# Optimization experiments

Hardware: AMD Instinct MI355X
Metric: run time of the kernel (lower is better)

The kernel has to match this reference:

```python
import jax, jax.numpy as jnp
import numpy as np

SPEC_WINDOW = 32
SPEC_HOP = 8
PELT_PENALTY = 3.0
PATCH_MIN = 8
PATCH_MAX = 64
PATCH_GRID = 2
ANCHOR_LEN = 16
ALPHA = 1.0
BETA = 1.0


def _spectral_batch_np(segs):
    # segs: [N, L] -> (feat [N,3], dom_period [N], bandwidth [N])
    segs = np.asarray(segs, dtype=np.float64)
    n, L = segs.shape
    if L < 2:
        return (np.zeros((n, 3), np.float32), np.ones(n, np.float32), np.zeros(n, np.float32))
    power = np.abs(np.fft.rfft(segs, axis=-1)) ** 2
    p = power[:, 1:]  # drop DC
    if p.shape[1] < 1:
        return (np.zeros((n, 3), np.float32), np.ones(n, np.float32), np.zeros(n, np.float32))
    total = p.sum(-1)
    probs = p / (total[:, None] + 1e-12)
    K = p.shape[1]
    freqs = np.arange(1, K + 1, dtype=np.float64) / L
    centroid = (probs * freqs).sum(-1)
    spread = np.sqrt(np.maximum((probs * (freqs - centroid[:, None]) ** 2).sum(-1), 0.0))
    dom_idx = p.argmax(-1)
    dom_period = L / (dom_idx + 1.0)
    bandwidth = 2.0 * spread  # normalized spectral spread
    feat = np.stack([centroid, bandwidth, np.log1p(total / L)], -1)
    return feat.astype(np.float32), dom_period.astype(np.float32), bandwidth.astype(np.float32)


def _dp_changepoints(feat, penalty):
    # penalized least-squares segmentation over window features
    feat = np.asarray(feat, np.float64)
    n, d = feat.shape
    cs = np.vstack([np.zeros((1, d)), np.cumsum(feat, 0)])
    cs2 = np.vstack([np.zeros((1, d)), np.cumsum(feat * feat, 0)])
    Fv = np.full(n + 1, np.inf)
    Fv[0] = 0.0
    parent = np.zeros(n + 1, np.int64)
    for t in range(1, n + 1):
        seglen = np.arange(t, 0, -1, dtype=np.float64)
        ds = cs[t] - cs[:t]
        ds2 = cs2[t] - cs2[:t]
        cost = ds2.sum(-1) - (ds * ds).sum(-1) / seglen
        vals = Fv[:t] + cost + penalty
        j = int(np.argmin(vals))
        Fv[t] = vals[j]
        parent[t] = j
    b = [n]
    t = n
    while t > 0:
        t = int(parent[t])
        b.append(t)
    return b[::-1]


def _detect_boundaries(agg):
    L = agg.shape[0]
    if L <= max(2, PATCH_MIN):
        return [0, L]
    window = min(SPEC_WINDOW, L)
    if L <= window:
        starts = [0]
        wins = agg[None, :]
    else:
        wins = np.lib.stride_tricks.sliding_window_view(agg, window)[::SPEC_HOP]
        starts = list(range(0, L - window + 1, SPEC_HOP))
        if starts[-1] != L - window:
            starts.append(L - window)
            wins = np.concatenate([wins, agg[None, -window:]], 0)
    feat, _, _ = _spectral_batch_np(wins)
    if feat.shape[0] <= 1:
        return [0, L]
    wb = _dp_changepoints(feat, PELT_PENALTY)
    bounds = [0]
    for w in wb[1:-1]:
        if w < 0 or w >= len(starts):
            continue
        t_idx = int(starts[w])
        if t_idx <= bounds[-1]:
            continue
        if t_idx - bounds[-1] < PATCH_MIN:
            continue
        if L - t_idx < PATCH_MIN:
            continue
        bounds.append(t_idx)
    bounds.append(L)
    return bounds


def _segment_stats(seg):
    if seg.shape[0] < 2:
        return 1.0, 0.0
    _, dp, bw = _spectral_batch_np(seg[None, :])
    return float(dp[0]), float(bw[0])


def _gen_patch_len(dom_period, bandwidth, seg_len):
    raw = ALPHA * dom_period / (1.0 + BETA * bandwidth)
    p = int(round(raw / PATCH_GRID)) * PATCH_GRID
    return max(1, max(PATCH_MIN, min(PATCH_MAX, p)))


def _plan_sample(series):
    # series: np [C, L]; returns (ops, starts, ends, regimes)
    C, L = series.shape
    agg = series.mean(0)
    bounds = _detect_boundaries(agg)
    ops = []
    starts = []
    ends = []
    regimes = []
    for s, e in zip(bounds[:-1], bounds[1:]):
        if e <= s:
            continue
        dp, bw = _segment_stats(agg[s:e])
        pl = _gen_patch_len(dp, bw, e - s)
        regime = (dp / max(L, 1), bw, (e - s) / max(L, 1))
        n_full = (e - s) // pl
        full_len = n_full * pl
        if n_full > 0:
            ops.append(("full", s, n_full, pl))
            starts += [s + i * pl for i in range(n_full)]
            ends += [s + (i + 1) * pl for i in range(n_full)]
            regimes += [regime] * n_full
        if full_len < e - s:
            ops.append(("tail", s + full_len, e))
            starts.append(s + full_len)
            ends.append(e)
            regimes.append(regime)
    if not ops:
        dp, bw = _segment_stats(agg)
        ops.append(("tail", 0, L))
        starts = [0]
        ends = [L]
        regimes = [(dp / max(L, 1), bw, 1.0)]
    return ops, np.asarray(starts, np.int64), np.asarray(ends, np.int64), np.asarray(regimes, np.float32)


def _lin_resize(arr, out_len):
    # matches F.interpolate(mode='linear', align_corners=False) on last dim
    P = arr.shape[-1]
    if P == out_len:
        return arr
    pos = (jnp.arange(out_len, dtype=jnp.float32) + 0.5) * (P / out_len) - 0.5
    pos = jnp.clip(pos, 0.0, P - 1)
    i0 = jnp.floor(pos).astype(jnp.int32)
    i1 = jnp.minimum(i0 + 1, P - 1)
    w = (pos - i0.astype(jnp.float32)).astype(arr.dtype)
    return arr[..., i0] * (1 - w) + arr[..., i1] * w


def _extract(xb, ops):
    # xb: jnp [C, L] -> [n_tokens, C, ANCHOR_LEN]
    C = xb.shape[0]
    chunks = []
    for op in ops:
        if op[0] == "full":
            _, s, n_full, pl = op
            full = xb[:, s:s + n_full * pl].reshape(C, n_full, pl).transpose(1, 0, 2)
            chunks.append(_lin_resize(full, ANCHOR_LEN))
        else:
            _, s, e = op
            chunks.append(_lin_resize(xb[:, s:e], ANCHOR_LEN)[None])
    return jnp.concatenate(chunks, 0)


def setup_inputs() -> dict:
    key = jax.random.key(0)
    x = jax.random.normal(key, (32, 64, 8192), dtype=jnp.float32)
    return {"x": x}


def reference(x):
    B, C, L = x.shape
    x_np = np.asarray(x)
    plans = [_plan_sample(x_np[b]) for b in range(B)]
    n_tok = [p[1].shape[0] for p in plans]
    N = max(n_tok)
    dc = float(max(L - 1, 1))
    ds = float(max(L, 1))
    patches = jnp.zeros((B, N, C, ANCHOR_LEN), jnp.float32)
    mask = np.zeros((B, N), bool)
    so = np.zeros((B, N), np.int64)
    eo = np.zeros((B, N), np.int64)
    co = np.zeros((B, N, 1), np.float32)
    sp = np.zeros((B, N, 1), np.float32)
    rg = np.zeros((B, N, 3), np.float32)
    for b, (ops, st, en, regime) in enumerate(plans):
        pb = _extract(x[b], ops)
        n = st.shape[0]
        patches = patches.at[b, :n].set(pb)
        mask[b, :n] = True
        so[b, :n] = st
        eo[b, :n] = en
        co[b, :n, 0] = ((st + en - 1.0) * 0.5 / dc).astype(np.float32)
        sp[b, :n, 0] = ((en - st) / ds).astype(np.float32)
        rg[b, :n] = regime
    return (patches, jnp.asarray(mask), jnp.asarray(so), jnp.asarray(eo), jnp.asarray(co), jnp.asarray(sp), jnp.asarray(rg), jnp.asarray(np.asarray(n_tok, np.int64)))
```

## Files before the change

kernel.cpp:

```cpp
#include <hip/hip_runtime.h>
#include <math.h>

#define BB 32
#define CC 64
#define LL 8192
#define WIN 32
#define HOP 8
#define NW 1021
#define NT 1022
#define NBINS 4096
#define SEGSTRIDE 1024
#define OFFSTRIDE 1025
#define MAXTOK 2048
#define ANCH 16
#define TWO_PI 6.283185307179586476925286766559
#define DP_TILE 64
#define DP_WAVES 8

__global__ void k_agg(const float* __restrict__ x, float* __restrict__ agg) {
  int idx = blockIdx.x * blockDim.x + threadIdx.x;
  if (idx >= BB * LL) return;
  int b = idx / LL, l = idx - b * LL;
  const float* xp = x + (size_t)b * CC * LL + l;
  float acc = 0.0f;
  for (int c = 0; c < CC; ++c) acc += xp[(size_t)c * LL];
  agg[idx] = acc / 64.0f;
}

__global__ void k_winfeat(const float* __restrict__ agg, float* __restrict__ feat) {
  __shared__ double ct[32], st[32];
  int b = blockIdx.x;
  int w = blockIdx.y * blockDim.x + threadIdx.x;
  if (threadIdx.x < 32) {
    double ang = -TWO_PI * (double)threadIdx.x / 32.0;
    sincos(ang, &st[threadIdx.x], &ct[threadIdx.x]);
  }
  __syncthreads();
  if (w >= NW) return;
  const float* a = agg + b * LL + w * HOP;
  double p[17];
  for (int k = 1; k <= 16; ++k) {
    double re = 0.0, im = 0.0;
    int m = 0;
    for (int n = 0; n < 32; ++n) {
      double av = (double)a[n];
      re += av * ct[m];
      im += av * st[m];
      m = (m + k) & 31;
    }
    p[k] = re * re + im * im;
  }
  double r[8];
  for (int j = 0; j < 8; ++j) r[j] = p[1 + j] + p[9 + j];
  double total = ((r[0] + r[1]) + (r[2] + r[3])) + ((r[4] + r[5]) + (r[6] + r[7]));
  double denom = total + 1e-12;
  double probs[17];
  for (int k = 1; k <= 16; ++k) probs[k] = p[k] / denom;
  for (int j = 0; j < 8; ++j)
    r[j] = probs[1 + j] * ((double)(1 + j) / 32.0) + probs[9 + j] * ((double)(9 + j) / 32.0);
  double centroid = ((r[0] + r[1]) + (r[2] + r[3])) + ((r[4] + r[5]) + (r[6] + r[7]));
  for (int j = 0; j < 8; ++j) {
    double f0 = (double)(1 + j) / 32.0 - centroid;
    double f1 = (double)(9 + j) / 32.0 - centroid;
    r[j] = probs[1 + j] * (f0 * f0) + probs[9 + j] * (f1 * f1);
  }
  double var = ((r[0] + r[1]) + (r[2] + r[3])) + ((r[4] + r[5]) + (r[6] + r[7]));
  double spread = sqrt(fmax(var, 0.0));
  size_t fo = ((size_t)b * 1024 + w) * 3;
  feat[fo + 0] = (float)centroid;
  feat[fo + 1] = (float)(2.0 * spread);
  feat[fo + 2] = (float)log1p(total / 32.0);
}

__global__ void __launch_bounds__(512)
k_dp(const float* __restrict__ feat,
     int* __restrict__ seg_s, int* __restrict__ seg_e,
     int* __restrict__ nsegp, int* __restrict__ segoff, int* __restrict__ binseg) {
  int b = blockIdx.x, tid = threadIdx.x;
  int wv = tid >> 6, lane = tid & 63;
  __shared__ double cs[NT][3];
  __shared__ double q[NT];
  __shared__ double G[NT];
  __shared__ short parent[NT];
  __shared__ int soff[OFFSTRIDE];
  __shared__ double redv[DP_WAVES][DP_TILE];
  __shared__ int redi[DP_WAVES][DP_TILE];
  __shared__ int ns_sh;

  if (tid == 0) {
    cs[0][0] = 0.0; cs[0][1] = 0.0; cs[0][2] = 0.0;
    q[0] = 0.0; G[0] = 0.0;
  }
  if (tid < 6) {
    int d = tid % 3; bool sq = tid >= 3;
    double acc = 0.0;
    for (int i = 0; i < NW; ++i) {
      double v = (double)feat[((size_t)b * 1024 + i) * 3 + d];
      acc += sq ? v * v : v;
      if (!sq) cs[i + 1][d] = acc;
      double a4 = __shfl(acc, 4);
      double a5 = __shfl(acc, 5);
      if (tid == 3) q[i + 1] = (acc + a4) + a5;
    }
  }
  __syncthreads();

  const int ntiles = (NW + DP_TILE - 1) / DP_TILE;
  for (int g = 0; g < ntiles; ++g) {
    int T0 = g * DP_TILE;
    int tcount = NW - T0; if (tcount > DP_TILE) tcount = DP_TILE;
    int t = T0 + 1 + lane;
    bool tvalid = lane < tcount;
    double ct0 = 0.0, ct1 = 0.0, ct2 = 0.0, Qt3 = 0.0;
    if (tvalid) { ct0 = cs[t][0]; ct1 = cs[t][1]; ct2 = cs[t][2]; Qt3 = q[t] + 3.0; }

    int njp = T0 + 1;
    int chunk = (njp + DP_WAVES - 1) / DP_WAVES;
    int j0 = wv * chunk;
    int j1 = j0 + chunk; if (j1 > njp) j1 = njp;
    double bv = INFINITY; int bj = 0x7fffffff;
    for (int j = j0; j < j1; ++j) {
      double c0 = cs[j][0], c1 = cs[j][1], c2 = cs[j][2], Gj = G[j];
      double d0 = ct0 - c0, d1 = ct1 - c1, d2 = ct2 - c2;
      double dd = (d0 * d0 + d1 * d1) + d2 * d2;
      double val = (Gj + Qt3) - dd / (double)(t - j);
      if (val < bv) { bv = val; bj = j; }
    }
    redv[wv][lane] = bv; redi[wv][lane] = bj;
    __syncthreads();

    if (wv == 0) {
      bv = redv[0][lane]; bj = redi[0][lane];
      for (int w = 1; w < DP_WAVES; ++w) {
        double ov = redv[w][lane]; int oj = redi[w][lane];
        if (ov < bv || (ov == bv && oj < bj)) { bv = ov; bj = oj; }
      }
      for (int l2 = 0; l2 < tcount - 1; ++l2) {
        double Gj_self = bv - (Qt3 - 3.0);
        double Gj  = __shfl(Gj_self, l2);
        double cj0 = __shfl(ct0, l2);
        double cj1 = __shfl(ct1, l2);
        double cj2 = __shfl(ct2, l2);
        if (tvalid && lane > l2) {
          double d0 = ct0 - cj0, d1 = ct1 - cj1, d2 = ct2 - cj2;
          double dd = (d0 * d0 + d1 * d1) + d2 * d2;
          double val = (Gj + Qt3) - dd / (double)(lane - l2);
          if (val < bv) { bv = val; bj = T0 + 1 + l2; }
        }
      }
      if (tvalid) { parent[t] = (short)bj; G[t] = bv - (Qt3 - 3.0); }
    }
    __syncthreads();
  }

  if (tid == 0) {
    short* path = (short*)&q[0];
    int* sb = (int*)&G[0];
    int cnt = 0, t = NW;
    while (t > 0) { t = parent[t]; path[cnt++] = (short)t; }
    int nb = 0, prev = 0;
    sb[nb++] = 0;
    for (int i = cnt - 2; i >= 0; --i) {
      int w = path[i];
      int ti = w * HOP;
      if (ti <= prev) continue;
      if (ti - prev < 8) continue;
      if (LL - ti < 8) continue;
      sb[nb++] = ti; prev = ti;
    }
    sb[nb++] = LL;
    int ns = nb - 1;
    ns_sh = ns;
    nsegp[b] = ns;
    int off = 0;
    for (int i = 0; i < ns; ++i) { soff[i] = off; off += (sb[i + 1] - sb[i]) >> 1; }
    soff[ns] = off;
  }
  __syncthreads();
  int ns = ns_sh;
  const int* sb = (const int*)&G[0];
  for (int i = tid; i < ns; i += 512) {
    seg_s[b * SEGSTRIDE + i] = sb[i];
    seg_e[b * SEGSTRIDE + i] = sb[i + 1];
    segoff[b * OFFSTRIDE + i] = soff[i];
    int o0 = soff[i], o1 = soff[i + 1];
    for (int qq = o0; qq < o1; ++qq) binseg[b * NBINS + qq] = i;
  }
  if (tid == 0) segoff[b * OFFSTRIDE + ns] = soff[ns];
}

__global__ void __launch_bounds__(256)
k_power(const float* __restrict__ agg,
        const int* __restrict__ seg_s, const int* __restrict__ seg_e,
        const int* __restrict__ segoff, const int* __restrict__ binseg,
        double* __restrict__ powb) {
  int gid = blockIdx.x * 256 + threadIdx.x;
  int lane8 = gid & 7;
  int bino = gid >> 3;
  int b = bino >> 12;
  int bin = bino & (NBINS - 1);
  int seg = binseg[b * NBINS + bin];
  int s = seg_s[b * SEGSTRIDE + seg];
  int e = seg_e[b * SEGSTRIDE + seg];
  int Ls = e - s;
  int k = bin - segoff[b * OFFSTRIDE + seg] + 1;
  const float* a = agg + b * LL + s;
  double wr, wi;
  sincos(-TWO_PI * (double)(8 * k) / (double)Ls, &wi, &wr);
  double cr, ci;
  sincos(-TWO_PI * (double)(k * lane8) / (double)Ls, &ci, &cr);
  double re = 0.0, im = 0.0;
  int j = 0;
  for (int n = lane8; n < Ls; n += 8, ++j) {
    if ((j & 63) == 0 && j) {
      int m = (int)(((long long)k * n) % Ls);
      sincos(-TWO_PI * (double)m / (double)Ls, &ci, &cr);
    }
    double av = (double)a[n];
    re = fma(av, cr, re);
    im = fma(av, ci, im);
    double nr = cr * wr - ci * wi;
    ci = fma(cr, wi, ci * wr);
    cr = nr;
  }
  for (int off = 4; off; off >>= 1) {
    re += __shfl_down(re, off, 8);
    im += __shfl_down(im, off, 8);
  }
  if (lane8 == 0) powb[(size_t)b * NBINS + bin] = re * re + im * im;
}

__global__ void k_segstat(const double* __restrict__ powb,
                          const int* __restrict__ seg_s, const int* __restrict__ seg_e,
                          const int* __restrict__ segoff, const int* __restrict__ nsegp,
                          float* __restrict__ dpv, float* __restrict__ bwv,
                          int* __restrict__ plv, int* __restrict__ ntokv) {
  int b = blockIdx.x, sidx = blockIdx.y;
  if (sidx >= nsegp[b]) return;
  int lane = threadIdx.x;
  int s = seg_s[b * SEGSTRIDE + sidx], e = seg_e[b * SEGSTRIDE + sidx];
  int Ls = e - s;
  int K = Ls >> 1;
  const double* p = powb + (size_t)b * NBINS + segoff[b * OFFSTRIDE + sidx];
  double T = 0.0, mx = -1.0; int mi = 0x7fffffff;
  for (int j = lane; j < K; j += 64) {
    double pv = p[j];
    T += pv;
    if (pv > mx) { mx = pv; mi = j; }
  }
  for (int off = 32; off > 0; off >>= 1) {
    T += __shfl_down(T, off);
    double omx = __shfl_down(mx, off);
    int omi = __shfl_down(mi, off);
    if (omx > mx || (omx == mx && omi < mi)) { mx = omx; mi = omi; }
  }
  T = __shfl(T, 0); mi = __shfl(mi, 0);
  double denom = T + 1e-12;
  double cp = 0.0;
  for (int j = lane; j < K; j += 64) cp += p[j] * ((double)(j + 1) / (double)Ls);
  for (int off = 32; off > 0; off >>= 1) cp += __shfl_down(cp, off);
  double c = __shfl(cp, 0) / denom;
  double sp2 = 0.0;
  for (int j = lane; j < K; j += 64) {
    double d = (double)(j + 1) / (double)Ls - c;
    sp2 += p[j] * (d * d);
  }
  for (int off = 32; off > 0; off >>= 1) sp2 += __shfl_down(sp2, off);
  if (lane == 0) {
    double spread = sqrt(fmax(sp2 / denom, 0.0));
    float dp32 = (float)((double)Ls / ((double)mi + 1.0));
    float bw32 = (float)(2.0 * spread);
    double raw = (double)dp32 / (1.0 + (double)bw32);
    int pl = (int)rint(raw * 0.5) * 2;
    pl = pl < 8 ? 8 : (pl > 64 ? 64 : pl);
    int nf = Ls / pl;
    dpv[b * SEGSTRIDE + sidx] = dp32;
    bwv[b * SEGSTRIDE + sidx] = bw32;
    plv[b * SEGSTRIDE + sidx] = pl;
    ntokv[b * SEGSTRIDE + sidx] = nf + ((nf * pl < Ls) ? 1 : 0);
  }
}

__global__ void k_plan(const int* __restrict__ nsegp, const int* __restrict__ ntokv,
                       const int* __restrict__ plv,
                       const int* __restrict__ seg_s, const int* __restrict__ seg_e,
                       int* __restrict__ tok_st, int* __restrict__ tok_en,
                       int* __restrict__ tok_sg, int* __restrict__ ntok,
                       float* __restrict__ out_ntok) {
  int b = blockIdx.x, tid = threadIdx.x;
  __shared__ int toff[SEGSTRIDE];
  int ns = nsegp[b];
  if (tid == 0) {
    int acc = 0;
    for (int i = 0; i < ns; ++i) { toff[i] = acc; acc += ntokv[b * SEGSTRIDE + i]; }
    if (acc > MAXTOK) acc = MAXTOK;
    ntok[b] = acc;
    out_ntok[b] = (float)acc;
  }
  __syncthreads();
  for (int i = tid; i < ns; i += blockDim.x) {
    int base = toff[i];
    int s = seg_s[b * SEGSTRIDE + i], e = seg_e[b * SEGSTRIDE + i];
    int pl = plv[b * SEGSTRIDE + i];
    int Ls = e - s;
    int nf = Ls / pl;
    for (int t = 0; t < nf; ++t) {
      int g = base + t;
      if (g >= MAXTOK) break;
      tok_st[b * MAXTOK + g] = s + t * pl;
      tok_en[b * MAXTOK + g] = s + (t + 1) * pl;
      tok_sg[b * MAXTOK + g] = i;
    }
    if (nf * pl < Ls) {
      int g = base + nf;
      if (g < MAXTOK) {
        tok_st[b * MAXTOK + g] = s + nf * pl;
        tok_en[b * MAXTOK + g] = e;
        tok_sg[b * MAXTOK + g] = i;
      }
    }
  }
}

__global__ void k_meta(const int* __restrict__ ntok,
                       const int* __restrict__ tok_st, const int* __restrict__ tok_en,
                       const int* __restrict__ tok_sg,
                       const float* __restrict__ dpv, const float* __restrict__ bwv,
                       const int* __restrict__ seg_s, const int* __restrict__ seg_e,
                       float* __restrict__ out, int N) {
  int idx = blockIdx.x * blockDim.x + threadIdx.x;
  if (idx >= BB * N) return;
  int b = idx / N, n = idx - b * N;
  float mask = 0, so = 0, eo = 0, co = 0, sp = 0, r0 = 0, r1 = 0, r2 = 0;
  if (n < ntok[b]) {
    int st = tok_st[b * MAXTOK + n], en = tok_en[b * MAXTOK + n], sg = tok_sg[b * MAXTOK + n];
    mask = 1.0f;
    so = (float)st; eo = (float)en;
    co = (float)(((double)st + (double)en - 1.0) * 0.5 / 8191.0);
    sp = (float)((double)(en - st) / 8192.0);
    r0 = (float)((double)dpv[b * SEGSTRIDE + sg] / 8192.0);
    r1 = bwv[b * SEGSTRIDE + sg];
    r2 = (float)((double)(seg_e[b * SEGSTRIDE + sg] - seg_s[b * SEGSTRIDE + sg]) / 8192.0);
  }
  size_t Nz = (size_t)N;
  size_t o1 = (size_t)32768 * Nz;
  out[o1 + idx] = mask;
  out[o1 + 32 * Nz + idx] = so;
  out[o1 + 64 * Nz + idx] = eo;
  out[o1 + 96 * Nz + idx] = co;
  out[o1 + 128 * Nz + idx] = sp;
  size_t o6 = o1 + 160 * Nz;
  out[o6 + (size_t)idx * 3 + 0] = r0;
  out[o6 + (size_t)idx * 3 + 1] = r1;
  out[o6 + (size_t)idx * 3 + 2] = r2;
}

__global__ void k_patches(const float* __restrict__ x,
                          const int* __restrict__ ntok,
                          const int* __restrict__ tok_st, const int* __restrict__ tok_en,
                          float* __restrict__ out, int N) {
  int blk = blockIdx.x;
  int b = blk / N, n = blk - b * N;
  size_t obase = (size_t)blk * (CC * ANCH);
  if (n >= ntok[b]) {
    for (int i = threadIdx.x; i < CC * ANCH; i += blockDim.x) out[obase + i] = 0.0f;
    return;
  }
  int st = tok_st[b * MAXTOK + n], en = tok_en[b * MAXTOK + n];
  int P = en - st;
  float scale = (float)((double)P / 16.0);
  float hi = (float)(P - 1);
  const float* xb = x + (size_t)b * CC * LL + st;
  for (int i = threadIdx.x; i < CC * ANCH; i += blockDim.x) {
    int c = i >> 4, k = i & 15;
    float pos = ((float)k + 0.5f) * scale - 0.5f;
    pos = fminf(fmaxf(pos, 0.0f), hi);
    int i0 = (int)floorf(pos);
    int i1 = min(i0 + 1, P - 1);
    float wgt = pos - (float)i0;
    const float* row = xb + (size_t)c * LL;
    out[obase + i] = row[i0] * (1.0f - wgt) + row[i1] * wgt;
  }
}

extern "C" void kernel_launch(void* const* d_in, const int* in_sizes, int n_in,
                              void* d_out, int out_size, void* d_ws, size_t ws_size,
                              hipStream_t stream) {
  const float* x = (const float*)d_in[0];
  float* out = (float*)d_out;
  int N = (out_size - BB) / 33024;
  if (N <= 0) return;

  char* ws = (char*)d_ws;
  size_t o = 0;
  auto A = [&](size_t bytes) { size_t r = o; o += (bytes + 255) & ~(size_t)255; return r; };
  float*  agg    = (float*) (ws + A((size_t)BB * LL * 4));
  float*  feat   = (float*) (ws + A((size_t)BB * 1024 * 3 * 4));
  int*    seg_s  = (int*)   (ws + A((size_t)BB * SEGSTRIDE * 4));
  int*    seg_e  = (int*)   (ws + A((size_t)BB * SEGSTRIDE * 4));
  int*    segoff = (int*)   (ws + A((size_t)BB * OFFSTRIDE * 4));
  int*    binseg = (int*)   (ws + A((size_t)BB * NBINS * 4));
  int*    nsegp  = (int*)   (ws + A((size_t)BB * 4));
  double* powb   = (double*)(ws + A((size_t)BB * NBINS * 8));
  float*  dpv    = (float*) (ws + A((size_t)BB * SEGSTRIDE * 4));
  float*  bwv    = (float*) (ws + A((size_t)BB * SEGSTRIDE * 4));
  int*    plv    = (int*)   (ws + A((size_t)BB * SEGSTRIDE * 4));
  int*    ntokv  = (int*)   (ws + A((size_t)BB * SEGSTRIDE * 4));
  int*    tok_st = (int*)   (ws + A((size_t)BB * MAXTOK * 4));
  int*    tok_en = (int*)   (ws + A((size_t)BB * MAXTOK * 4));
  int*    tok_sg = (int*)   (ws + A((size_t)BB * MAXTOK * 4));
  int*    ntok   = (int*)   (ws + A((size_t)BB * 4));
  (void)ws_size; (void)in_sizes; (void)n_in;

  k_agg<<<dim3((BB * LL + 255) / 256), dim3(256), 0, stream>>>(x, agg);
  k_winfeat<<<dim3(BB, (NW + 255) / 256), dim3(256), 0, stream>>>(agg, feat);
  k_dp<<<dim3(BB), dim3(512), 0, stream>>>(feat, seg_s, seg_e, nsegp, segoff, binseg);
  k_power<<<dim3(BB * NBINS * 8 / 256), dim3(256), 0, stream>>>(agg, seg_s, seg_e, segoff, binseg, powb);
  k_segstat<<<dim3(BB, SEGSTRIDE), dim3(64), 0, stream>>>(powb, seg_s, seg_e, segoff, nsegp,
                                                          dpv, bwv, plv, ntokv);
  k_plan<<<dim3(BB), dim3(256), 0, stream>>>(nsegp, ntokv, plv, seg_s, seg_e,
                                             tok_st, tok_en, tok_sg, ntok,
                                             out + (size_t)33024 * N);
  k_meta<<<dim3((BB * N + 255) / 256), dim3(256), 0, stream>>>(ntok, tok_st, tok_en, tok_sg,
                                                               dpv, bwv, seg_s, seg_e, out, N);
  k_patches<<<dim3(BB * N), dim3(256), 0, stream>>>(x, ntok, tok_st, tok_en, out, N);
}
```

Before: 1.408 ms.

## Split segment DFT into radix-8 sub-DFTs plus twiddle combine pass

Replaces the direct per-bin DFT over each segment with a two-stage radix-8 decimation-in-time scheme. The first kernel computes length-Ls/8 DFTs of each residue class, and the second combines the eight sub-results with twiddles per bin. This cuts the trig-recurrence arithmetic per bin by roughly the radix factor. In exchange it adds a per-sample segment map, an extra workspace buffer and launch, and relies on segment lengths being multiples of eight. It falls back to the old kernel when the workspace is too small.

```diff
diff --git a/kernel.cpp b/kernel.cpp
--- a/kernel.cpp
+++ b/kernel.cpp
@@ -75,7 +75,8 @@
 __global__ void __launch_bounds__(512)
 k_dp(const float* __restrict__ feat,
      int* __restrict__ seg_s, int* __restrict__ seg_e,
-     int* __restrict__ nsegp, int* __restrict__ segoff, int* __restrict__ binseg) {
+     int* __restrict__ nsegp, int* __restrict__ segoff, int* __restrict__ binseg,
+     int* __restrict__ smap) {
   int b = blockIdx.x, tid = threadIdx.x;
   int wv = tid >> 6, lane = tid & 63;
   __shared__ double cs[NT][3];
@@ -185,15 +186,18 @@
     segoff[b * OFFSTRIDE + i] = soff[i];
     int o0 = soff[i], o1 = soff[i + 1];
     for (int qq = o0; qq < o1; ++qq) binseg[b * NBINS + qq] = i;
+    if (smap) {
+      for (int p = sb[i]; p < sb[i + 1]; ++p) smap[b * LL + p] = i;
+    }
   }
   if (tid == 0) segoff[b * OFFSTRIDE + ns] = soff[ns];
 }
 
 __global__ void __launch_bounds__(256)
-k_power(const float* __restrict__ agg,
-        const int* __restrict__ seg_s, const int* __restrict__ seg_e,
-        const int* __restrict__ segoff, const int* __restrict__ binseg,
-        double* __restrict__ powb) {
+k_power8(const float* __restrict__ agg,
+         const int* __restrict__ seg_s, const int* __restrict__ seg_e,
+         const int* __restrict__ segoff, const int* __restrict__ binseg,
+         double* __restrict__ powb) {
   int gid = blockIdx.x * 256 + threadIdx.x;
   int lane8 = gid & 7;
   int bino = gid >> 3;
@@ -230,6 +234,77 @@
   if (lane8 == 0) powb[(size_t)b * NBINS + bin] = re * re + im * im;
 }
 
+__global__ void __launch_bounds__(256)
+k_power1(const float* __restrict__ agg,
+         const int* __restrict__ seg_s, const int* __restrict__ seg_e,
+         const int* __restrict__ smap,
+         double* __restrict__ sub) {
+  int gid = blockIdx.x * 256 + threadIdx.x;
+  int lane8 = gid & 7;
+  int po = gid >> 3;
+  int b = po >> 13;
+  int p = po & (LL - 1);
+  int seg = smap[b * LL + p];
+  int s = seg_s[b * SEGSTRIDE + seg];
+  int Ls = seg_e[b * SEGSTRIDE + seg] - s;
+  int M = Ls >> 3;
+  int i = p - s;
+  int q = i >> 3, r = i & 7;
+  const float* a = agg + b * LL + s;
+  double wr, wi;
+  sincos(-TWO_PI * (double)(8 * q) / (double)M, &wi, &wr);
+  double cr, ci;
+  sincos(-TWO_PI * (double)(q * lane8) / (double)M, &ci, &cr);
+  double re = 0.0, im = 0.0;
+  int j = 0;
+  for (int m = lane8; m < M; m += 8, ++j) {
+    if ((j & 63) == 0 && j) {
+      int mm = (int)(((long long)q * m) % M);
+      sincos(-TWO_PI * (double)mm / (double)M, &ci, &cr);
+    }
+    double av = (double)a[(m << 3) + r];
+    re = fma(av, cr, re);
+    im = fma(av, ci, im);
+    double nr = cr * wr - ci * wi;
+    ci = fma(cr, wi, ci * wr);
+    cr = nr;
+  }
+  for (int off = 4; off; off >>= 1) {
+    re += __shfl_down(re, off, 8);
+    im += __shfl_down(im, off, 8);
+  }
+  if (lane8 == 0) {
+    size_t o = ((size_t)b * LL + p) * 2;
+    sub[o] = re; sub[o + 1] = im;
+  }
+}
+
+__global__ void __launch_bounds__(256)
+k_power2(const double* __restrict__ sub,
+         const int* __restrict__ seg_s, const int* __restrict__ seg_e,
+         const int* __restrict__ segoff, const int* __restrict__ binseg,
+         double* __restrict__ powb) {
+  int gid = blockIdx.x * 256 + threadIdx.x;
+  int b = gid >> 12;
+  int bin = gid & (NBINS - 1);
+  int seg = binseg[b * NBINS + bin];
+  int s = seg_s[b * SEGSTRIDE + seg];
+  int Ls = seg_e[b * SEGSTRIDE + seg] - s;
+  int M = Ls >> 3;
+  int k = bin - segoff[b * OFFSTRIDE + seg] + 1;
+  int q0 = k - (k / M) * M;
+  const double* S = sub + ((size_t)b * LL + s + q0 * 8) * 2;
+  double wr, wi;
+  sincos(-TWO_PI * (double)k / (double)Ls, &wi, &wr);
+  double xr = S[14], xi = S[15];
+  for (int r = 6; r >= 0; --r) {
+    double nr = (xr * wr - xi * wi) + S[2 * r];
+    xi = (xr * wi + xi * wr) + S[2 * r + 1];
+    xr = nr;
+  }
+  powb[(size_t)b * NBINS + bin] = xr * xr + xi * xi;
+}
+
 __global__ void k_segstat(const double* __restrict__ powb,
                           const int* __restrict__ seg_s, const int* __restrict__ seg_e,
                           const int* __restrict__ segoff, const int* __restrict__ nsegp,
@@ -410,12 +485,21 @@
   int*    tok_en = (int*)   (ws + A((size_t)BB * MAXTOK * 4));
   int*    tok_sg = (int*)   (ws + A((size_t)BB * MAXTOK * 4));
   int*    ntok   = (int*)   (ws + A((size_t)BB * 4));
-  (void)ws_size; (void)in_sizes; (void)n_in;
+  int*    smap   = (int*)   (ws + A((size_t)BB * LL * 4));
+  double* sub    = (double*)(ws + A((size_t)BB * LL * 2 * 8));
+  bool use_r8 = (o <= ws_size);
+  (void)in_sizes; (void)n_in;
 
   k_agg<<<dim3((BB * LL + 255) / 256), dim3(256), 0, stream>>>(x, agg);
   k_winfeat<<<dim3(BB, (NW + 255) / 256), dim3(256), 0, stream>>>(agg, feat);
-  k_dp<<<dim3(BB), dim3(512), 0, stream>>>(feat, seg_s, seg_e, nsegp, segoff, binseg);
-  k_power<<<dim3(BB * NBINS * 8 / 256), dim3(256), 0, stream>>>(agg, seg_s, seg_e, segoff, binseg, powb);
+  k_dp<<<dim3(BB), dim3(512), 0, stream>>>(feat, seg_s, seg_e, nsegp, segoff, binseg,
+                                           use_r8 ? smap : (int*)nullptr);
+  if (use_r8) {
+    k_power1<<<dim3(BB * LL * 8 / 256), dim3(256), 0, stream>>>(agg, seg_s, seg_e, smap, sub);
+    k_power2<<<dim3(BB * NBINS / 256), dim3(256), 0, stream>>>(sub, seg_s, seg_e, segoff, binseg, powb);
+  } else {
+    k_power8<<<dim3(BB * NBINS * 8 / 256), dim3(256), 0, stream>>>(agg, seg_s, seg_e, segoff, binseg, powb);
+  }
   k_segstat<<<dim3(BB, SEGSTRIDE), dim3(64), 0, stream>>>(powb, seg_s, seg_e, segoff, nsegp,
                                                           dpv, bwv, plv, ntokv);
   k_plan<<<dim3(BB), dim3(256), 0, stream>>>(nsegp, ntokv, plv, seg_s, seg_e,
```

Result: faster. 1.268 ms (-10.0%).
